# Optimization experiments

Hardware: AMD Instinct MI355X
Metric: run time of the kernel (lower is better)

The kernel has to match this reference:

```python
import jax, jax.numpy as jnp
import numpy as np

M_CHK, N_VAR, DV = 576, 1152, 3  # (3,x)-regular-column LDPC, rate 1/2
PI = 3.1415926


def _build_bp_matrices():
    """Vectorized replica of GetMatrixForBPNet (same math, no Python O(E^2) loops)."""
    rng = np.random.default_rng(0)
    H = np.zeros((M_CHK, N_VAR), np.float32)
    rows = np.argsort(rng.random((N_VAR, M_CHK)), axis=1)[:, :DV]  # DV distinct rows per column
    H[rows.ravel(), np.repeat(np.arange(N_VAR), DV)] = 1.0
    ii, jj = np.nonzero(H)                 # row-major edge list (sorted by row, then col)
    E = ii.size
    p_r2l = np.lexsort((ii, jj))           # Map_row_to_line: col-major position -> row-major index
    p_l2r = np.argsort(p_r2l)              # Map_line_to_row: inverse permutation
    cols_cm = jj[p_r2l]                    # column of each edge in col-major ("line") order
    # variable-node sum excluding self, in col-major order, then permute row-major input -> col-major
    S_V = (cols_cm[:, None] == cols_cm[None, :]).astype(np.float32)
    np.fill_diagonal(S_V, 0.0)
    H_sumV_to_C = np.zeros((E, E), np.float32)
    H_sumV_to_C[:, p_r2l] = S_V
    # check-node sum excluding self, in row-major order, then permute col-major input -> row-major
    S_C = (ii[:, None] == ii[None, :]).astype(np.float32)
    np.fill_diagonal(S_C, 0.0)
    H_sumC_to_V = np.zeros((E, E), np.float32)
    H_sumC_to_V[:, p_l2r] = S_C
    # llr -> per-edge init (col-major order)
    H_x_to_xe0 = np.zeros((E, N_VAR), np.float32)
    H_x_to_xe0[np.arange(E), cols_cm] = 1.0
    # per-variable sum of final edge messages (row-major input -> col-major sum)
    A = (np.arange(N_VAR)[:, None] == cols_cm[None, :]).astype(np.float32)
    H_xe_v_sumc_to_y = np.zeros((N_VAR, E), np.float32)
    H_xe_v_sumc_to_y[:, p_r2l] = A
    return H_x_to_xe0, H_sumC_to_V, H_sumV_to_C, H_xe_v_sumc_to_y


def setup_inputs() -> dict:
    key = jax.random.key(0)
    H_x_to_xe0, H_sumC_to_V, H_sumV_to_C, H_xe_v_sumc_to_y = _build_bp_matrices()
    llr_in = 2.0 * jax.random.normal(key, (16, N_VAR), dtype=jnp.float32)
    return {
        "llr_in": llr_in,
        "H_x_to_xe0": jnp.asarray(H_x_to_xe0),
        "H_sumC_to_V": jnp.asarray(H_sumC_to_V),
        "H_sumV_to_C": jnp.asarray(H_sumV_to_C),
        "H_xe_v_sumc_to_y": jnp.asarray(H_xe_v_sumc_to_y),
        "bp_iter_num": 8,
    }


def _one_bp_iteration(xe_v2c, xe_0, H_sumC_to_V, H_sumV_to_C):
    xe_tanh = jnp.tanh(xe_v2c / 2.0)
    sgn = jnp.sign(xe_tanh)
    # log-domain product over check-node neighbors (excluding self) via complex log trick
    sum_log_img = H_sumC_to_V @ ((1.0 - sgn) * (0.5 * PI))
    sum_log_real = H_sumC_to_V @ jnp.log(1e-8 + jnp.abs(xe_tanh))
    xe_product = jnp.exp(sum_log_real) * jnp.cos(sum_log_img)  # Re(exp(r + i*theta))
    xe_pd = xe_product + jnp.sign(xe_product) * (-2e-7)
    # 2 * atanh(x) with the module's custom atanh = 0.5*log((1+x)/(1-x+1e-10))
    xe_v_sumc = jnp.log((1.0 + xe_pd) / (1.0 - xe_pd + 1e-10))
    xe_c_sumv = xe_0 + H_sumV_to_C @ xe_v_sumc
    return xe_v_sumc, xe_c_sumv


def reference(llr_in, H_x_to_xe0, H_sumC_to_V, H_sumV_to_C, H_xe_v_sumc_to_y, bp_iter_num):
    llr_t = llr_in.T                      # [n, batch]
    xe_0 = H_x_to_xe0 @ llr_t             # [E, batch]
    xe_v2c = xe_0
    for _ in range(bp_iter_num - 1):
        _, xe_v2c = _one_bp_iteration(xe_v2c, xe_0, H_sumC_to_V, H_sumV_to_C)
    xe_v_sumc, _ = _one_bp_iteration(xe_v2c, xe_0, H_sumC_to_V, H_sumV_to_C)
    bp_out_llr = llr_t + H_xe_v_sumc_to_y @ xe_v_sumc
    dec_out = (1 - jnp.sign(bp_out_llr).astype(jnp.int32)) // 2
    return dec_out.T
```

## Files before the change

kernel.cpp:

```cpp
#include <hip/hip_runtime.h>

#define NV 1152
#define MC 576
#define NE 3456

__global__ __launch_bounds__(256) void k_tri(const float* __restrict__ Hy,
                                             unsigned short* __restrict__ pl2r) {
    __shared__ int found[8];
    __shared__ int fcnt;
    const int v = blockIdx.x, t = threadIdx.x;
    if (t == 0) fcnt = 0;
    __syncthreads();
    const float4* row4 = (const float4*)(Hy + (size_t)v * NE);
    for (int c4 = t; c4 < 864; c4 += 256) {
        float4 q = row4[c4];
        if (q.x != 0.0f) { int s = atomicAdd(&fcnt, 1); if (s < 8) found[s] = 4 * c4; }
        if (q.y != 0.0f) { int s = atomicAdd(&fcnt, 1); if (s < 8) found[s] = 4 * c4 + 1; }
        if (q.z != 0.0f) { int s = atomicAdd(&fcnt, 1); if (s < 8) found[s] = 4 * c4 + 2; }
        if (q.w != 0.0f) { int s = atomicAdd(&fcnt, 1); if (s < 8) found[s] = 4 * c4 + 3; }
    }
    __syncthreads();
    if (t == 0) {
        int a = found[0], b2 = found[1], c2 = found[2];
        int lo = min(a, min(b2, c2));
        int hi = max(a, max(b2, c2));
        int mid = a + b2 + c2 - lo - hi;
        pl2r[lo]  = (unsigned short)(3 * v);
        pl2r[mid] = (unsigned short)(3 * v + 1);
        pl2r[hi]  = (unsigned short)(3 * v + 2);
    }
}

__global__ __launch_bounds__(1024) void k_build(const float* __restrict__ Hc,
                                                const unsigned short* __restrict__ pl2r,
                                                int* __restrict__ rs) {
    __shared__ unsigned short flg[NE];
    __shared__ int wtot[16];
    const int t = threadIdx.x;
    const int lane = t & 63, wid = t >> 6;
    for (int r = t; r < MC + 1; r += 1024) rs[r] = NE;
    for (int a = t; a < NE; a += 1024) {
        int fl = 0;
        if (a > 0) fl = (Hc[(size_t)(a - 1) * NE + (int)pl2r[a]] == 0.0f) ? 1 : 0;
        flg[a] = (unsigned short)fl;
    }
    __syncthreads();
    int inc[4];
    int run = 0;
    const int base4 = t * 4;
    #pragma unroll
    for (int k = 0; k < 4; k++) {
        int idx = base4 + k;
        run += (idx < NE) ? (int)flg[idx] : 0;
        inc[k] = run;
    }
    int x = run;
    #pragma unroll
    for (int d = 1; d < 64; d <<= 1) {
        int y = __shfl_up(x, d, 64);
        if (lane >= d) x += y;
    }
    if (lane == 63) wtot[wid] = x;
    __syncthreads();
    if (t < 16) {
        int v = wtot[t];
        #pragma unroll
        for (int d = 1; d < 16; d <<= 1) {
            int y = __shfl_up(v, d, 16);
            if (t >= d) v += y;
        }
        wtot[t] = v;
    }
    __syncthreads();
    const int prefix = ((wid > 0) ? wtot[wid - 1] : 0) + (x - run);
    #pragma unroll
    for (int k = 0; k < 4; k++) {
        int idx = base4 + k;
        if (idx < NE) {
            int rid = prefix + inc[k];
            if (idx == 0 || flg[idx]) rs[rid] = idx;
        }
    }
}

__global__ __launch_bounds__(1024) void k_main(const float* __restrict__ llr,
                                               const unsigned short* __restrict__ pl2r,
                                               const int* __restrict__ rs,
                                               int* __restrict__ out) {
    __shared__ int rsl[MC + 1];
    __shared__ unsigned short ecm[NE];
    __shared__ unsigned short rloc[NE];
    __shared__ float llr_s[NV];
    __shared__ float msg[NE];
    __shared__ float2 lrli[NE];
    const int b = blockIdx.x, t = threadIdx.x;

    for (int r = t; r < MC + 1; r += 1024) rsl[r] = rs[r];
    for (int v = t; v < NV; v += 1024) llr_s[v] = llr[b * NV + v];
    for (int a = t; a < NE; a += 1024) ecm[a] = pl2r[a];
    __syncthreads();
    for (int a = t; a < NE; a += 1024) {
        int lo = 0, hi = MC - 1;
        while (lo < hi) { int mid = (lo + hi + 1) >> 1; if (rsl[mid] <= a) lo = mid; else hi = mid - 1; }
        rloc[a] = (unsigned short)lo;
    }
    __syncthreads();

    for (int it = 0; it < 8; ++it) {
        for (int a = t; a < NE; a += 1024) {
            int e = ecm[a];
            int v = e / 3;
            float xv = llr_s[v];
            if (it > 0) {
                int v3 = 3 * v, r_ = e - v3;
                int o1 = v3 + ((r_ == 0) ? 1 : 0);
                int o2 = v3 + ((r_ == 2) ? 1 : 2);
                xv = xv + (msg[o1] + msg[o2]);
            }
            float tv = tanhf(0.5f * xv);
            float sgn = (tv > 0.0f) ? 1.0f : ((tv < 0.0f) ? -1.0f : 0.0f);
            lrli[a] = make_float2(logf(1e-8f + fabsf(tv)),
                                  (1.0f - sgn) * 1.5707963f);
        }
        __syncthreads();
        for (int a = t; a < NE; a += 1024) {
            int r = rloc[a];
            int js = rsl[r], je = rsl[r + 1];
            float slr = 0.0f, sli = 0.0f;
            for (int j = js; j < je; ++j) {
                if (j != a) { float2 q = lrli[j]; slr += q.x; sli += q.y; }
            }
            float p = expf(slr) * cosf(sli);
            float ps = (p > 0.0f) ? 1.0f : ((p < 0.0f) ? -1.0f : 0.0f);
            float pd = p - 2e-7f * ps;
            msg[ecm[a]] = logf((1.0f + pd) / ((1.0f - pd) + 1e-10f));
        }
        __syncthreads();
    }

    for (int v = t; v < NV; v += 1024) {
        float S = (msg[3 * v] + msg[3 * v + 1]) + msg[3 * v + 2];
        out[b * NV + v] = ((llr_s[v] + S) < 0.0f) ? 1 : 0;
    }
}

extern "C" void kernel_launch(void* const* d_in, const int* in_sizes, int n_in,
                              void* d_out, int out_size, void* d_ws, size_t ws_size,
                              hipStream_t stream) {
    const float* llr_in = (const float*)d_in[0];
    const float* Hc2v   = (const float*)d_in[2];
    const float* Hy     = (const float*)d_in[4];
    const int batch = in_sizes[0] / NV;

    int* rs = (int*)d_ws;
    unsigned short* pl2r = (unsigned short*)(rs + 580);

    hipLaunchKernelGGL(k_tri, dim3(NV), dim3(256), 0, stream, Hy, pl2r);
    hipLaunchKernelGGL(k_build, dim3(1), dim3(1024), 0, stream, Hc2v, pl2r, rs);
    hipLaunchKernelGGL(k_main, dim3(batch), dim3(1024), 0, stream,
                       llr_in, pl2r, rs, llr_in ? (int*)d_out : (int*)d_out);
}
```

Measured before the change: 195.3 us.

## Assign check rows per wavefront and double-buffer messages to drop a barrier

Measured after the change: 200.5 us. 2.7% more time.

```diff
diff --git a/kernel.cpp b/kernel.cpp
--- a/kernel.cpp
+++ b/kernel.cpp
@@ -3,6 +3,7 @@
 #define NV 1152
 #define MC 576
 #define NE 3456
+#define RPW 36
 
 __global__ __launch_bounds__(256) void k_tri(const float* __restrict__ Hy,
                                              unsigned short* __restrict__ pl2r) {
@@ -87,59 +88,71 @@
                                                const unsigned short* __restrict__ pl2r,
                                                const int* __restrict__ rs,
                                                int* __restrict__ out) {
-    __shared__ int rsl[MC + 1];
-    __shared__ unsigned short ecm[NE];
-    __shared__ unsigned short rloc[NE];
+    __shared__ float m0[NE];
+    __shared__ float m1[NE];
+    __shared__ float slr_s[NE];
+    __shared__ unsigned short ecm_s[NE];
+    __shared__ unsigned short js_s[NE];
+    __shared__ unsigned char len_s[NE];
     __shared__ float llr_s[NV];
-    __shared__ float msg[NE];
-    __shared__ float2 lrli[NE];
     const int b = blockIdx.x, t = threadIdx.x;
+    const int lane = t & 63, wid = t >> 6;
+    int* rsl = (int*)slr_s;
 
     for (int r = t; r < MC + 1; r += 1024) rsl[r] = rs[r];
     for (int v = t; v < NV; v += 1024) llr_s[v] = llr[b * NV + v];
-    for (int a = t; a < NE; a += 1024) ecm[a] = pl2r[a];
+    for (int a = t; a < NE; a += 1024) ecm_s[a] = pl2r[a];
     __syncthreads();
+    const int s0w = rsl[wid * RPW];
+    const int s1w = rsl[wid * RPW + RPW];
     for (int a = t; a < NE; a += 1024) {
         int lo = 0, hi = MC - 1;
         while (lo < hi) { int mid = (lo + hi + 1) >> 1; if (rsl[mid] <= a) lo = mid; else hi = mid - 1; }
-        rloc[a] = (unsigned short)lo;
+        int js = rsl[lo], je = rsl[lo + 1];
+        js_s[a] = (unsigned short)js;
+        len_s[a] = (unsigned char)(je - js);
     }
     __syncthreads();
 
     for (int it = 0; it < 8; ++it) {
-        for (int a = t; a < NE; a += 1024) {
-            int e = ecm[a];
+        const float* mp = (it & 1) ? m1 : m0;
+        float* mn       = (it & 1) ? m0 : m1;
+        for (int a = s0w + lane; a < s1w; a += 64) {
+            int e = ecm_s[a] & 0xFFF;
             int v = e / 3;
             float xv = llr_s[v];
             if (it > 0) {
                 int v3 = 3 * v, r_ = e - v3;
                 int o1 = v3 + ((r_ == 0) ? 1 : 0);
                 int o2 = v3 + ((r_ == 2) ? 1 : 2);
-                xv = xv + (msg[o1] + msg[o2]);
+                xv = xv + (mp[o1] + mp[o2]);
             }
             float tv = tanhf(0.5f * xv);
-            float sgn = (tv > 0.0f) ? 1.0f : ((tv < 0.0f) ? -1.0f : 0.0f);
-            lrli[a] = make_float2(logf(1e-8f + fabsf(tv)),
-                                  (1.0f - sgn) * 1.5707963f);
+            int code = (tv > 0.0f) ? 0 : ((tv < 0.0f) ? 2 : 1);
+            slr_s[a] = logf(1e-8f + fabsf(tv));
+            ecm_s[a] = (unsigned short)(e | (code << 12));
         }
-        __syncthreads();
-        for (int a = t; a < NE; a += 1024) {
-            int r = rloc[a];
-            int js = rsl[r], je = rsl[r + 1];
+        asm volatile("s_waitcnt lgkmcnt(0)" ::: "memory");
+        for (int a = s0w + lane; a < s1w; a += 64) {
+            int e = ecm_s[a] & 0xFFF;
+            int js = js_s[a], je = js + (int)len_s[a];
             float slr = 0.0f, sli = 0.0f;
             for (int j = js; j < je; ++j) {
-                if (j != a) { float2 q = lrli[j]; slr += q.x; sli += q.y; }
+                if (j != a) {
+                    slr += slr_s[j];
+                    sli += 1.5707963f * (float)(ecm_s[j] >> 12);
+                }
             }
             float p = expf(slr) * cosf(sli);
             float ps = (p > 0.0f) ? 1.0f : ((p < 0.0f) ? -1.0f : 0.0f);
             float pd = p - 2e-7f * ps;
-            msg[ecm[a]] = logf((1.0f + pd) / ((1.0f - pd) + 1e-10f));
+            mn[e] = logf((1.0f + pd) / ((1.0f - pd) + 1e-10f));
         }
         __syncthreads();
     }
 
     for (int v = t; v < NV; v += 1024) {
-        float S = (msg[3 * v] + msg[3 * v + 1]) + msg[3 * v + 2];
+        float S = (m0[3 * v] + m0[3 * v + 1]) + m0[3 * v + 2];
         out[b * NV + v] = ((llr_s[v] + S) < 0.0f) ? 1 : 0;
     }
 }
@@ -158,5 +171,5 @@
     hipLaunchKernelGGL(k_tri, dim3(NV), dim3(256), 0, stream, Hy, pl2r);
     hipLaunchKernelGGL(k_build, dim3(1), dim3(1024), 0, stream, Hc2v, pl2r, rs);
     hipLaunchKernelGGL(k_main, dim3(batch), dim3(1024), 0, stream,
-                       llr_in, pl2r, rs, llr_in ? (int*)d_out : (int*)d_out);
+                       llr_in, pl2r, rs, (int*)d_out);
 }
```

## Split BP iterations into per-iteration kernels over check-row groups and batch

Applied to the files above, without the earlier changes.

Result: faster. 175.4 us (-10.2%).

```diff
diff --git a/kernel.cpp b/kernel.cpp
--- a/kernel.cpp
+++ b/kernel.cpp
@@ -3,6 +3,9 @@
 #define NV 1152
 #define MC 576
 #define NE 3456
+#define RPG 36
+#define GRP 16
+#define EMAX 384
 
 __global__ __launch_bounds__(256) void k_tri(const float* __restrict__ Hy,
                                              unsigned short* __restrict__ pl2r) {
@@ -33,12 +36,14 @@
 
 __global__ __launch_bounds__(1024) void k_build(const float* __restrict__ Hc,
                                                 const unsigned short* __restrict__ pl2r,
-                                                int* __restrict__ rs) {
+                                                int* __restrict__ rs,
+                                                uint2* __restrict__ etab) {
     __shared__ unsigned short flg[NE];
     __shared__ int wtot[16];
+    __shared__ int rsl[MC + 1];
     const int t = threadIdx.x;
     const int lane = t & 63, wid = t >> 6;
-    for (int r = t; r < MC + 1; r += 1024) rs[r] = NE;
+    for (int r = t; r < MC + 1; r += 1024) rsl[r] = NE;
     for (int a = t; a < NE; a += 1024) {
         int fl = 0;
         if (a > 0) fl = (Hc[(size_t)(a - 1) * NE + (int)pl2r[a]] == 0.0f) ? 1 : 0;
@@ -78,70 +83,73 @@
         int idx = base4 + k;
         if (idx < NE) {
             int rid = prefix + inc[k];
-            if (idx == 0 || flg[idx]) rs[rid] = idx;
+            if (idx == 0 || flg[idx]) rsl[rid] = idx;
+        }
+    }
+    __syncthreads();
+    for (int r = t; r < MC + 1; r += 1024) rs[r] = rsl[r];
+    #pragma unroll
+    for (int k = 0; k < 4; k++) {
+        int a = base4 + k;
+        if (a < NE) {
+            int r = prefix + inc[k];
+            int js = rsl[r];
+            int len = rsl[r + 1] - js;
+            int jsr = js - rsl[(r / RPG) * RPG];
+            int e = pl2r[a];
+            int v3 = 3 * (e / 3), r_ = e - v3;
+            int o1 = v3 + ((r_ == 0) ? 1 : 0);
+            int o2 = v3 + ((r_ == 2) ? 1 : 2);
+            etab[a] = make_uint2((unsigned)(e | (jsr << 16)),
+                                 (unsigned)(o1 | (o2 << 12) | (len << 24)));
         }
     }
 }
 
-__global__ __launch_bounds__(1024) void k_main(const float* __restrict__ llr,
-                                               const unsigned short* __restrict__ pl2r,
+__global__ __launch_bounds__(EMAX) void k_iter(const float* __restrict__ llr,
+                                               const uint2* __restrict__ etab,
                                                const int* __restrict__ rs,
-                                               int* __restrict__ out) {
-    __shared__ int rsl[MC + 1];
-    __shared__ unsigned short ecm[NE];
-    __shared__ unsigned short rloc[NE];
-    __shared__ float llr_s[NV];
-    __shared__ float msg[NE];
-    __shared__ float2 lrli[NE];
-    const int b = blockIdx.x, t = threadIdx.x;
-
-    for (int r = t; r < MC + 1; r += 1024) rsl[r] = rs[r];
-    for (int v = t; v < NV; v += 1024) llr_s[v] = llr[b * NV + v];
-    for (int a = t; a < NE; a += 1024) ecm[a] = pl2r[a];
-    __syncthreads();
-    for (int a = t; a < NE; a += 1024) {
-        int lo = 0, hi = MC - 1;
-        while (lo < hi) { int mid = (lo + hi + 1) >> 1; if (rsl[mid] <= a) lo = mid; else hi = mid - 1; }
-        rloc[a] = (unsigned short)lo;
+                                               const float* __restrict__ mi,
+                                               float* __restrict__ mo,
+                                               int first) {
+    __shared__ float2 lrli[EMAX];
+    const int g = blockIdx.x, b = blockIdx.y, t = threadIdx.x;
+    const int s0 = rs[g * RPG], s1 = rs[g * RPG + RPG];
+    const int n = s1 - s0;
+    int e = 0, jsr = 0, len = 0, o1, o2;
+    if (t < n) {
+        uint2 u = etab[s0 + t];
+        e   = u.x & 0xFFFF;  jsr = u.x >> 16;
+        o1  = u.y & 0xFFF;   o2  = (u.y >> 12) & 0xFFF;  len = u.y >> 24;
+        float xv = llr[b * NV + e / 3];
+        if (!first) xv = xv + (mi[b * NE + o1] + mi[b * NE + o2]);
+        float tv = tanhf(0.5f * xv);
+        float sgn = (tv > 0.0f) ? 1.0f : ((tv < 0.0f) ? -1.0f : 0.0f);
+        lrli[t] = make_float2(logf(1e-8f + fabsf(tv)),
+                              (1.0f - sgn) * 1.5707963f);
     }
     __syncthreads();
+    if (t < n) {
+        float slr = 0.0f, sli = 0.0f;
+        const int je = jsr + len;
+        for (int j = jsr; j < je; ++j) {
+            if (j != t) { float2 q = lrli[j]; slr += q.x; sli += q.y; }
+        }
+        float p = expf(slr) * cosf(sli);
+        float ps = (p > 0.0f) ? 1.0f : ((p < 0.0f) ? -1.0f : 0.0f);
+        float pd = p - 2e-7f * ps;
+        mo[b * NE + e] = logf((1.0f + pd) / ((1.0f - pd) + 1e-10f));
+    }
+}
 
-    for (int it = 0; it < 8; ++it) {
-        for (int a = t; a < NE; a += 1024) {
-            int e = ecm[a];
-            int v = e / 3;
-            float xv = llr_s[v];
-            if (it > 0) {
-                int v3 = 3 * v, r_ = e - v3;
-                int o1 = v3 + ((r_ == 0) ? 1 : 0);
-                int o2 = v3 + ((r_ == 2) ? 1 : 2);
-                xv = xv + (msg[o1] + msg[o2]);
-            }
-            float tv = tanhf(0.5f * xv);
-            float sgn = (tv > 0.0f) ? 1.0f : ((tv < 0.0f) ? -1.0f : 0.0f);
-            lrli[a] = make_float2(logf(1e-8f + fabsf(tv)),
-                                  (1.0f - sgn) * 1.5707963f);
-        }
-        __syncthreads();
-        for (int a = t; a < NE; a += 1024) {
-            int r = rloc[a];
-            int js = rsl[r], je = rsl[r + 1];
-            float slr = 0.0f, sli = 0.0f;
-            for (int j = js; j < je; ++j) {
-                if (j != a) { float2 q = lrli[j]; slr += q.x; sli += q.y; }
-            }
-            float p = expf(slr) * cosf(sli);
-            float ps = (p > 0.0f) ? 1.0f : ((p < 0.0f) ? -1.0f : 0.0f);
-            float pd = p - 2e-7f * ps;
-            msg[ecm[a]] = logf((1.0f + pd) / ((1.0f - pd) + 1e-10f));
-        }
-        __syncthreads();
-    }
-
-    for (int v = t; v < NV; v += 1024) {
-        float S = (msg[3 * v] + msg[3 * v + 1]) + msg[3 * v + 2];
-        out[b * NV + v] = ((llr_s[v] + S) < 0.0f) ? 1 : 0;
-    }
+__global__ void k_out(const float* __restrict__ llr, const float* __restrict__ msg,
+                      int* __restrict__ out, int n) {
+    int i = blockIdx.x * 256 + threadIdx.x;
+    if (i >= n) return;
+    int b = i / NV, v = i - b * NV;
+    const float* m = msg + (size_t)b * NE + 3 * v;
+    float S = (m[0] + m[1]) + m[2];
+    out[i] = ((llr[i] + S) < 0.0f) ? 1 : 0;
 }
 
 extern "C" void kernel_launch(void* const* d_in, const int* in_sizes, int n_in,
@@ -154,9 +162,22 @@
 
     int* rs = (int*)d_ws;
     unsigned short* pl2r = (unsigned short*)(rs + 580);
+    uint2* etab = (uint2*)(pl2r + NE);
+    float* msgA = (float*)(etab + NE);
+    float* msgB = msgA + (size_t)batch * NE;
 
     hipLaunchKernelGGL(k_tri, dim3(NV), dim3(256), 0, stream, Hy, pl2r);
-    hipLaunchKernelGGL(k_build, dim3(1), dim3(1024), 0, stream, Hc2v, pl2r, rs);
-    hipLaunchKernelGGL(k_main, dim3(batch), dim3(1024), 0, stream,
-                       llr_in, pl2r, rs, llr_in ? (int*)d_out : (int*)d_out);
+    hipLaunchKernelGGL(k_build, dim3(1), dim3(1024), 0, stream, Hc2v, pl2r, rs, etab);
+    hipLaunchKernelGGL(k_iter, dim3(GRP, batch), dim3(EMAX), 0, stream,
+                       llr_in, etab, rs, msgA, msgA, 1);
+    float* bufs[2] = { msgA, msgB };
+    for (int it = 1; it < 8; ++it) {
+        float* in  = bufs[(it + 1) & 1];
+        float* out = bufs[it & 1];
+        hipLaunchKernelGGL(k_iter, dim3(GRP, batch), dim3(EMAX), 0, stream,
+                           llr_in, etab, rs, in, out, 0);
+    }
+    const int n = batch * NV;
+    hipLaunchKernelGGL(k_out, dim3((n + 255) / 256), dim3(256), 0, stream,
+                       llr_in, msgB, (int*)d_out, n);
 }
```
